# Kernel tuning notes

Hardware: AMD Instinct MI355X
Metric: run time of the kernel (lower is better)

## Reference

```python
import jax, jax.numpy as jnp
import numpy as np

MARGIN = 0.2
EPS = 1e-5
NEG_SENTINEL = -1e9


def _cos_sim(a, b):
    a = a / jnp.linalg.norm(a, axis=-1, keepdims=True)
    b = b / jnp.linalg.norm(b, axis=-1, keepdims=True)
    return a @ b.T  # [B, B]


def _row_losses(sm, labels):
    # sm: [B, B] similarity matrix; one loop body of the original, vectorized over rows i.
    diag = jnp.diagonal(sm)                      # pos_pair_ (scalar per row)
    pos_valid = diag < (1.0 - EPS)               # pos_pair_[pos_pair_ < 1-eps]
    neg_mask = labels[None, :] != labels[:, None]
    # neg_pair_[neg_pair_ + margin > min(pos_pair_)] ; min of a scalar is itself
    hard = neg_mask & ((sm + MARGIN) > diag[:, None])
    has_neg = jnp.any(hard, axis=1)
    neg_max = jnp.max(jnp.where(hard, sm, NEG_SENTINEL), axis=1)  # max(neg_pair)
    valid = pos_valid & has_neg
    pos_loss = jnp.maximum(0.2 * diag * diag - 0.7 * diag + 0.5, 0.0)
    neg_loss = jnp.maximum(0.9 * neg_max * neg_max - 0.4 * neg_max + 0.03, 0.0)
    return jnp.sum(jnp.where(valid, pos_loss + neg_loss, 0.0))


def setup_inputs() -> dict:
    key = jax.random.key(0)
    k1, k2 = jax.random.split(key)
    B, D = 8192, 256
    audio_embeds = jax.random.normal(k1, (B, D), dtype=jnp.float32)
    text_embeds = jax.random.normal(k2, (B, D), dtype=jnp.float32)
    labels = jnp.arange(B, dtype=jnp.int64)
    return {"audio_embeds": audio_embeds, "text_embeds": text_embeds, "labels": labels}


def reference(audio_embeds, text_embeds, labels):
    scores = _cos_sim(audio_embeds, text_embeds)  # [B, B]
    B = scores.shape[0]
    total = _row_losses(scores, labels) + _row_losses(scores.T, labels)
    return total / B
```

## Files before the change

kernel.cpp:

```cpp
#include <hip/hip_runtime.h>
#include <stdint.h>

#define BM 128
#define BN 128
#define KD 256

typedef __attribute__((ext_vector_type(4))) float f32x4;
typedef __attribute__((ext_vector_type(4))) int   i32x4;
typedef __attribute__((ext_vector_type(8))) int   i32x8;

__device__ __forceinline__ float fmax4(f32x4 v) {
  return fmaxf(fmaxf(v[0], v[1]), fmaxf(v[2], v[3]));
}

__global__ __launch_bounds__(256) void norm_kernel(
    const float* __restrict__ a, const float* __restrict__ b,
    unsigned int* __restrict__ an, unsigned int* __restrict__ bn,
    float* __restrict__ diag, float* __restrict__ out, int D) {
  if (blockIdx.x == 0 && threadIdx.x == 0) out[0] = 0.f;
  const int row = blockIdx.x * 4 + (threadIdx.x >> 6);
  const int l = threadIdx.x & 63;
  const float4 av = ((const float4*)(a + (size_t)row * D))[l];
  const float4 bv = ((const float4*)(b + (size_t)row * D))[l];
  float ssa = av.x*av.x + av.y*av.y + av.z*av.z + av.w*av.w;
  float ssb = bv.x*bv.x + bv.y*bv.y + bv.z*bv.z + bv.w*bv.w;
  float dot = av.x*bv.x + av.y*bv.y + av.z*bv.z + av.w*bv.w;
  for (int off = 1; off < 64; off <<= 1) {
    ssa += __shfl_xor(ssa, off, 64);
    ssb += __shfl_xor(ssb, off, 64);
    dot += __shfl_xor(dot, off, 64);
  }
  const float inva = 1.0f / sqrtf(ssa);
  const float invb = 1.0f / sqrtf(ssb);
  if (l == 0) diag[row] = dot * inva * invb;
  int pa = 0, pb = 0;
  pa = __builtin_amdgcn_cvt_pk_fp8_f32(av.x * inva, av.y * inva, pa, 0);
  pa = __builtin_amdgcn_cvt_pk_fp8_f32(av.z * inva, av.w * inva, pa, 1);
  pb = __builtin_amdgcn_cvt_pk_fp8_f32(bv.x * invb, bv.y * invb, pb, 0);
  pb = __builtin_amdgcn_cvt_pk_fp8_f32(bv.z * invb, bv.w * invb, pb, 1);
  an[(size_t)row * (D / 4) + l] = (unsigned int)pa;
  bn[(size_t)row * (D / 4) + l] = (unsigned int)pb;
}

__global__ __launch_bounds__(256, 4) void gemm_max_kernel(
    const unsigned char* __restrict__ an, const unsigned char* __restrict__ bn,
    const int* __restrict__ labels,
    float* __restrict__ row_part, float* __restrict__ col_part, int B) {
  __shared__ __align__(16) unsigned char sA[2][BM * 128];
  __shared__ float lds_col[2][BN];

  const int tid  = threadIdx.x;
  const int lane = tid & 63;
  const int w    = tid >> 6;
  const int wm   = w >> 1, wn = w & 1;
  const int tj   = blockIdx.x & 63;
  const int ti   = blockIdx.x >> 6;

  const int sr  = lane >> 3;
  const int sc8 = lane & 7;
  const int ssw = (sc8 ^ sr) * 16;
  #pragma unroll
  for (int it = 0; it < 2; ++it)
    #pragma unroll
    for (int c = 0; c < 4; ++c) {
      const int r0 = w * 32 + c * 8;
      const unsigned char* ga = an + (size_t)(ti * BM + r0 + sr) * KD + it * 128 + ssw;
      __builtin_amdgcn_global_load_lds(
          (const __attribute__((address_space(1))) void*)ga,
          (__attribute__((address_space(3))) void*)(&sA[it][r0 * 128] + lane * 16), 16, 0, 0);
    }

  const int fr = lane & 15;
  const int hi = lane >> 4;
  const int p0 = ((2 * hi)     ^ (fr & 7)) * 16;
  const int p1 = ((2 * hi + 1) ^ (fr & 7)) * 16;

  const unsigned char* gb = bn + (size_t)(tj * BN + wn * 64 + fr) * KD + hi * 32;

  f32x4 acc[4][4];
  #pragma unroll
  for (int mt = 0; mt < 4; ++mt)
    #pragma unroll
    for (int nt = 0; nt < 4; ++nt)
      acc[mt][nt] = (f32x4){0.f, 0.f, 0.f, 0.f};

  const int SC = 0x7F7F7F7F;

  __syncthreads();

  #pragma unroll 1
  for (int it = 0; it < 2; ++it) {
    const unsigned char* sAb = &sA[it][0];
    i32x8 af[4];
    #pragma unroll
    for (int mt = 0; mt < 4; ++mt) {
      const unsigned char* ra = sAb + (wm * 64 + mt * 16 + fr) * 128;
      i32x4 alo = *(const i32x4*)(ra + p0), ahi = *(const i32x4*)(ra + p1);
      af[mt] = __builtin_shufflevector(alo, ahi, 0, 1, 2, 3, 4, 5, 6, 7);
    }
    #pragma unroll
    for (int nt = 0; nt < 4; ++nt) {
      const i32x8 bf = *(const i32x8*)(gb + (size_t)nt * 16 * KD + it * 128);
      #pragma unroll
      for (int mt = 0; mt < 4; ++mt)
        acc[mt][nt] = __builtin_amdgcn_mfma_scale_f32_16x16x128_f8f6f4(
            af[mt], bf, acc[mt][nt], 0, 0, 0, SC, 0, SC);
    }
  }

  int li[4][4], labc[4];
  #pragma unroll
  for (int mt = 0; mt < 4; ++mt)
    #pragma unroll
    for (int r = 0; r < 4; ++r)
      li[mt][r] = labels[ti * BM + wm * 64 + mt * 16 + hi * 4 + r];
  #pragma unroll
  for (int nt = 0; nt < 4; ++nt)
    labc[nt] = labels[tj * BN + wn * 64 + nt * 16 + fr];

  float rp[4][4];
  float cp[4] = {-1e9f, -1e9f, -1e9f, -1e9f};
  #pragma unroll
  for (int mt = 0; mt < 4; ++mt)
    #pragma unroll
    for (int r = 0; r < 4; ++r) {
      const int l0 = li[mt][r];
      float rm = -1e9f;
      #pragma unroll
      for (int nt = 0; nt < 4; ++nt) {
        const float vm = (l0 != labc[nt]) ? acc[mt][nt][r] : -1e9f;
        rm = fmaxf(rm, vm);
        cp[nt] = fmaxf(cp[nt], vm);
      }
      rp[mt][r] = rm;
    }

  #pragma unroll
  for (int nt = 0; nt < 4; ++nt) {
    float c = cp[nt];
    c = fmaxf(c, __shfl_xor(c, 16, 64));
    c = fmaxf(c, __shfl_xor(c, 32, 64));
    if (hi == 0) lds_col[wm][wn * 64 + nt * 16 + fr] = c;
  }

  __syncthreads();

  float* red = (float*)&sA[0][0];
  const int s = wn * 16 + fr;
  #pragma unroll
  for (int mt = 0; mt < 4; ++mt)
    #pragma unroll
    for (int r = 0; r < 4; ++r) {
      const int i = wm * 64 + mt * 16 + hi * 4 + r;
      red[i * 32 + (((s >> 2) ^ (i & 7)) << 2) + (s & 3)] = rp[mt][r];
    }
  __syncthreads();

  if (tid < BM) {
    const int key = tid & 7;
    const f32x4* rr = (const f32x4*)(red + tid * 32);
    f32x4 m4 = rr[0 ^ key];
    #pragma unroll
    for (int k = 1; k < 8; ++k) {
      f32x4 v = rr[k ^ key];
      m4[0] = fmaxf(m4[0], v[0]); m4[1] = fmaxf(m4[1], v[1]);
      m4[2] = fmaxf(m4[2], v[2]); m4[3] = fmaxf(m4[3], v[3]);
    }
    row_part[(size_t)tj * B + ti * BM + tid] = fmax4(m4);
  } else if (tid < BM + BN) {
    const int t2 = tid - BM;
    col_part[(size_t)ti * B + tj * BN + t2] =
        fmaxf(lds_col[0][t2], lds_col[1][t2]);
  }
}

__global__ __launch_bounds__(256) void finalize_kernel(
    const float* __restrict__ row_part, const float* __restrict__ col_part,
    const float* __restrict__ diag, int B, int T, float* __restrict__ out) {
  const int v = blockIdx.x * 256 + threadIdx.x;
  const bool isrow = v < B;
  const int i = isrow ? v : v - B;
  const float* part = isrow ? row_part : col_part;
  float m = -1e9f;
  for (int t = 0; t < T; ++t) m = fmaxf(m, part[(size_t)t * B + i]);
  const float d = diag[i];
  float loss = 0.f;
  if ((d < 1.0f - 1e-5f) && (m + 0.2f > d)) {
    loss = fmaxf(0.2f * d * d - 0.7f * d + 0.5f, 0.f) +
           fmaxf(0.9f * m * m - 0.4f * m + 0.03f, 0.f);
  }
  for (int off = 1; off < 64; off <<= 1) loss += __shfl_xor(loss, off, 64);
  __shared__ float ssum[4];
  if ((threadIdx.x & 63) == 0) ssum[threadIdx.x >> 6] = loss;
  __syncthreads();
  if (threadIdx.x == 0)
    atomicAdd(out, (ssum[0] + ssum[1] + ssum[2] + ssum[3]) / (float)B);
}

extern "C" void kernel_launch(void* const* d_in, const int* in_sizes, int n_in,
                              void* d_out, int out_size, void* d_ws, size_t ws_size,
                              hipStream_t stream) {
  const float* a      = (const float*)d_in[0];
  const float* b      = (const float*)d_in[1];
  const int*   labels = (const int*)d_in[2];
  const int B = in_sizes[2];
  const int D = in_sizes[0] / B;
  const int T = B / BM;

  char* ws = (char*)d_ws;
  unsigned char* an = (unsigned char*)ws;
  unsigned char* bn = (unsigned char*)(ws + (size_t)B * D);
  float* diag     = (float*)(ws + (size_t)2 * B * D);
  float* row_part = diag + B;
  float* col_part = row_part + (size_t)T * B;

  norm_kernel<<<B / 4, 256, 0, stream>>>(a, b, (unsigned int*)an,
                                         (unsigned int*)bn, diag,
                                         (float*)d_out, D);

  gemm_max_kernel<<<(B / BM) * (B / BN), 256, 0, stream>>>(
      an, bn, labels, row_part, col_part, B);

  finalize_kernel<<<(2 * B) / 256, 256, 0, stream>>>(
      row_part, col_part, diag, B, T, (float*)d_out);
}
```

Baseline: 130.4 us.

## Keep A fragments in registers and loop over eight column tiles per block

Each block now loads its 128-row A tile once straight into registers, with no LDS staging, and iterates over eight 128-column B tiles. This amortizes the A loads and per-block setup across eight tiles. The LDS-based row/column reductions and block barriers are replaced by wave shuffles with direct per-wave writes of partial maxima. The grid shrinks from 4096 to 512 blocks, the occupancy hint drops to 2, and the column partials double, so finalize reads more data and fewer blocks are left to hide latency.

```diff
diff --git a/kernel.cpp b/kernel.cpp
--- a/kernel.cpp
+++ b/kernel.cpp
@@ -1,17 +1,10 @@
 #include <hip/hip_runtime.h>
 #include <stdint.h>
 
-#define BM 128
-#define BN 128
 #define KD 256
 
 typedef __attribute__((ext_vector_type(4))) float f32x4;
-typedef __attribute__((ext_vector_type(4))) int   i32x4;
 typedef __attribute__((ext_vector_type(8))) int   i32x8;
-
-__device__ __forceinline__ float fmax4(f32x4 v) {
-  return fmaxf(fmaxf(v[0], v[1]), fmaxf(v[2], v[3]));
-}
 
 __global__ __launch_bounds__(256) void norm_kernel(
     const float* __restrict__ a, const float* __restrict__ b,
@@ -42,145 +35,119 @@
   bn[(size_t)row * (D / 4) + l] = (unsigned int)pb;
 }
 
-__global__ __launch_bounds__(256, 4) void gemm_max_kernel(
+__global__ __launch_bounds__(256, 2) void gemm_max_kernel(
     const unsigned char* __restrict__ an, const unsigned char* __restrict__ bn,
     const int* __restrict__ labels,
     float* __restrict__ row_part, float* __restrict__ col_part, int B) {
-  __shared__ __align__(16) unsigned char sA[2][BM * 128];
-  __shared__ float lds_col[2][BN];
+  const int lane = threadIdx.x & 63;
+  const int w    = threadIdx.x >> 6;
+  const int wm   = w >> 1, wn = w & 1;
+  const int jg   = blockIdx.x & 7;
+  const int ti   = blockIdx.x >> 3;
+  const int fr   = lane & 15;
+  const int hi   = lane >> 4;
 
-  const int tid  = threadIdx.x;
-  const int lane = tid & 63;
-  const int w    = tid >> 6;
-  const int wm   = w >> 1, wn = w & 1;
-  const int tj   = blockIdx.x & 63;
-  const int ti   = blockIdx.x >> 6;
-
-  const int sr  = lane >> 3;
-  const int sc8 = lane & 7;
-  const int ssw = (sc8 ^ sr) * 16;
-  #pragma unroll
-  for (int it = 0; it < 2; ++it)
-    #pragma unroll
-    for (int c = 0; c < 4; ++c) {
-      const int r0 = w * 32 + c * 8;
-      const unsigned char* ga = an + (size_t)(ti * BM + r0 + sr) * KD + it * 128 + ssw;
-      __builtin_amdgcn_global_load_lds(
-          (const __attribute__((address_space(1))) void*)ga,
-          (__attribute__((address_space(3))) void*)(&sA[it][r0 * 128] + lane * 16), 16, 0, 0);
-    }
-
-  const int fr = lane & 15;
-  const int hi = lane >> 4;
-  const int p0 = ((2 * hi)     ^ (fr & 7)) * 16;
-  const int p1 = ((2 * hi + 1) ^ (fr & 7)) * 16;
-
-  const unsigned char* gb = bn + (size_t)(tj * BN + wn * 64 + fr) * KD + hi * 32;
-
-  f32x4 acc[4][4];
+  const unsigned char* ga = an + (size_t)(ti * 128 + wm * 64 + fr) * KD + hi * 32;
+  i32x8 af[4][2];
   #pragma unroll
   for (int mt = 0; mt < 4; ++mt)
     #pragma unroll
-    for (int nt = 0; nt < 4; ++nt)
-      acc[mt][nt] = (f32x4){0.f, 0.f, 0.f, 0.f};
+    for (int it = 0; it < 2; ++it)
+      af[mt][it] = *(const i32x8*)(ga + (size_t)(mt * 16) * KD + it * 128);
 
-  const int SC = 0x7F7F7F7F;
-
-  __syncthreads();
-
-  #pragma unroll 1
-  for (int it = 0; it < 2; ++it) {
-    const unsigned char* sAb = &sA[it][0];
-    i32x8 af[4];
-    #pragma unroll
-    for (int mt = 0; mt < 4; ++mt) {
-      const unsigned char* ra = sAb + (wm * 64 + mt * 16 + fr) * 128;
-      i32x4 alo = *(const i32x4*)(ra + p0), ahi = *(const i32x4*)(ra + p1);
-      af[mt] = __builtin_shufflevector(alo, ahi, 0, 1, 2, 3, 4, 5, 6, 7);
-    }
-    #pragma unroll
-    for (int nt = 0; nt < 4; ++nt) {
-      const i32x8 bf = *(const i32x8*)(gb + (size_t)nt * 16 * KD + it * 128);
-      #pragma unroll
-      for (int mt = 0; mt < 4; ++mt)
-        acc[mt][nt] = __builtin_amdgcn_mfma_scale_f32_16x16x128_f8f6f4(
-            af[mt], bf, acc[mt][nt], 0, 0, 0, SC, 0, SC);
-    }
-  }
-
-  int li[4][4], labc[4];
+  int li[4][4];
   #pragma unroll
   for (int mt = 0; mt < 4; ++mt)
     #pragma unroll
     for (int r = 0; r < 4; ++r)
-      li[mt][r] = labels[ti * BM + wm * 64 + mt * 16 + hi * 4 + r];
-  #pragma unroll
-  for (int nt = 0; nt < 4; ++nt)
-    labc[nt] = labels[tj * BN + wn * 64 + nt * 16 + fr];
+      li[mt][r] = labels[ti * 128 + wm * 64 + mt * 16 + hi * 4 + r];
 
   float rp[4][4];
-  float cp[4] = {-1e9f, -1e9f, -1e9f, -1e9f};
+  #pragma unroll
+  for (int mt = 0; mt < 4; ++mt)
+    #pragma unroll
+    for (int r = 0; r < 4; ++r) rp[mt][r] = -1e9f;
+
+  const int SC = 0x7F7F7F7F;
+  const f32x4 fz = {0.f, 0.f, 0.f, 0.f};
+
+  #pragma unroll 1
+  for (int t = 0; t < 8; ++t) {
+    const int tj = jg * 8 + t;
+    const unsigned char* gb = bn + (size_t)(tj * 128 + wn * 64 + fr) * KD + hi * 32;
+
+    int labc[4];
+    #pragma unroll
+    for (int nt = 0; nt < 4; ++nt)
+      labc[nt] = labels[tj * 128 + wn * 64 + nt * 16 + fr];
+
+    f32x4 acc[4][4];
+    #pragma unroll
+    for (int nt = 0; nt < 4; ++nt) {
+      const i32x8 bf = *(const i32x8*)(gb + (size_t)(nt * 16) * KD);
+      #pragma unroll
+      for (int mt = 0; mt < 4; ++mt)
+        acc[mt][nt] = __builtin_amdgcn_mfma_scale_f32_16x16x128_f8f6f4(
+            af[mt][0], bf, fz, 0, 0, 0, SC, 0, SC);
+    }
+    #pragma unroll
+    for (int nt = 0; nt < 4; ++nt) {
+      const i32x8 bf = *(const i32x8*)(gb + (size_t)(nt * 16) * KD + 128);
+      #pragma unroll
+      for (int mt = 0; mt < 4; ++mt)
+        acc[mt][nt] = __builtin_amdgcn_mfma_scale_f32_16x16x128_f8f6f4(
+            af[mt][1], bf, acc[mt][nt], 0, 0, 0, SC, 0, SC);
+    }
+
+    float cp[4] = {-1e9f, -1e9f, -1e9f, -1e9f};
+    #pragma unroll
+    for (int mt = 0; mt < 4; ++mt)
+      #pragma unroll
+      for (int r = 0; r < 4; ++r) {
+        const int l0 = li[mt][r];
+        float rm = rp[mt][r];
+        #pragma unroll
+        for (int nt = 0; nt < 4; ++nt) {
+          const float vm = (l0 != labc[nt]) ? acc[mt][nt][r] : -1e9f;
+          rm = fmaxf(rm, vm);
+          cp[nt] = fmaxf(cp[nt], vm);
+        }
+        rp[mt][r] = rm;
+      }
+
+    #pragma unroll
+    for (int nt = 0; nt < 4; ++nt) {
+      float c = cp[nt];
+      c = fmaxf(c, __shfl_xor(c, 16, 64));
+      c = fmaxf(c, __shfl_xor(c, 32, 64));
+      if (lane < 16)
+        col_part[(size_t)(ti * 2 + wm) * B + tj * 128 + wn * 64 + nt * 16 + fr] = c;
+    }
+  }
+
   #pragma unroll
   for (int mt = 0; mt < 4; ++mt)
     #pragma unroll
     for (int r = 0; r < 4; ++r) {
-      const int l0 = li[mt][r];
-      float rm = -1e9f;
+      float v = rp[mt][r];
       #pragma unroll
-      for (int nt = 0; nt < 4; ++nt) {
-        const float vm = (l0 != labc[nt]) ? acc[mt][nt][r] : -1e9f;
-        rm = fmaxf(rm, vm);
-        cp[nt] = fmaxf(cp[nt], vm);
-      }
-      rp[mt][r] = rm;
+      for (int off = 1; off < 16; off <<= 1)
+        v = fmaxf(v, __shfl_xor(v, off, 64));
+      if (fr == 0)
+        row_part[(size_t)(jg * 2 + wn) * B +
+                 ti * 128 + wm * 64 + mt * 16 + hi * 4 + r] = v;
     }
-
-  #pragma unroll
-  for (int nt = 0; nt < 4; ++nt) {
-    float c = cp[nt];
-    c = fmaxf(c, __shfl_xor(c, 16, 64));
-    c = fmaxf(c, __shfl_xor(c, 32, 64));
-    if (hi == 0) lds_col[wm][wn * 64 + nt * 16 + fr] = c;
-  }
-
-  __syncthreads();
-
-  float* red = (float*)&sA[0][0];
-  const int s = wn * 16 + fr;
-  #pragma unroll
-  for (int mt = 0; mt < 4; ++mt)
-    #pragma unroll
-    for (int r = 0; r < 4; ++r) {
-      const int i = wm * 64 + mt * 16 + hi * 4 + r;
-      red[i * 32 + (((s >> 2) ^ (i & 7)) << 2) + (s & 3)] = rp[mt][r];
-    }
-  __syncthreads();
-
-  if (tid < BM) {
-    const int key = tid & 7;
-    const f32x4* rr = (const f32x4*)(red + tid * 32);
-    f32x4 m4 = rr[0 ^ key];
-    #pragma unroll
-    for (int k = 1; k < 8; ++k) {
-      f32x4 v = rr[k ^ key];
-      m4[0] = fmaxf(m4[0], v[0]); m4[1] = fmaxf(m4[1], v[1]);
-      m4[2] = fmaxf(m4[2], v[2]); m4[3] = fmaxf(m4[3], v[3]);
-    }
-    row_part[(size_t)tj * B + ti * BM + tid] = fmax4(m4);
-  } else if (tid < BM + BN) {
-    const int t2 = tid - BM;
-    col_part[(size_t)ti * B + tj * BN + t2] =
-        fmaxf(lds_col[0][t2], lds_col[1][t2]);
-  }
 }
 
 __global__ __launch_bounds__(256) void finalize_kernel(
     const float* __restrict__ row_part, const float* __restrict__ col_part,
-    const float* __restrict__ diag, int B, int T, float* __restrict__ out) {
+    const float* __restrict__ diag, int B, int Trow, int Tcol,
+    float* __restrict__ out) {
   const int v = blockIdx.x * 256 + threadIdx.x;
   const bool isrow = v < B;
   const int i = isrow ? v : v - B;
   const float* part = isrow ? row_part : col_part;
+  const int T = isrow ? Trow : Tcol;
   float m = -1e9f;
   for (int t = 0; t < T; ++t) m = fmaxf(m, part[(size_t)t * B + i]);
   const float d = diag[i];
@@ -205,22 +172,23 @@
   const int*   labels = (const int*)d_in[2];
   const int B = in_sizes[2];
   const int D = in_sizes[0] / B;
-  const int T = B / BM;
+  const int Trow = 16;
+  const int Tcol = (B / 128) * 2;
 
   char* ws = (char*)d_ws;
   unsigned char* an = (unsigned char*)ws;
   unsigned char* bn = (unsigned char*)(ws + (size_t)B * D);
   float* diag     = (float*)(ws + (size_t)2 * B * D);
   float* row_part = diag + B;
-  float* col_part = row_part + (size_t)T * B;
+  float* col_part = row_part + (size_t)Trow * B;
 
   norm_kernel<<<B / 4, 256, 0, stream>>>(a, b, (unsigned int*)an,
                                          (unsigned int*)bn, diag,
                                          (float*)d_out, D);
 
-  gemm_max_kernel<<<(B / BM) * (B / BN), 256, 0, stream>>>(
+  gemm_max_kernel<<<(B / 128) * 8, 256, 0, stream>>>(
       an, bn, labels, row_part, col_part, B);
 
   finalize_kernel<<<(2 * B) / 256, 256, 0, stream>>>(
-      row_part, col_part, diag, B, T, (float*)d_out);
+      row_part, col_part, diag, B, Trow, Tcol, (float*)d_out);
 }
```

Result: slower. 141.0 us (+8.1%).
